# Kernel optimization log

Hardware: AMD Instinct MI355X
Metric: run time of the kernel (lower is better)

Reference implementation:

```python
import jax, jax.numpy as jnp
import numpy as np

B = 8192          # batch
DIM = 2048        # feature dim
FANOUT = 10       # balanced 10-ary tree, depth 3 -> 1000 leaves
N_NODES = 1 + 10 + 100  # inner nodes with classifiers = 111
NUM_CLASSES = 1000


def setup_inputs() -> dict:
    key = jax.random.key(0)
    k1, k2, k3, k4 = jax.random.split(key, 4)
    x = jax.random.normal(k1, (B, DIM), dtype=jnp.float32)
    labels = jax.random.randint(k2, (B,), 0, NUM_CLASSES, dtype=jnp.int64 if jax.config.jax_enable_x64 else jnp.int32)
    # Stacked per-node Linear(dim, num_child+1): column 0 is the extra slot
    # included in the softmax but never routed to (children use cols 1..FANOUT).
    W = jax.random.normal(k3, (N_NODES, DIM, FANOUT + 1), dtype=jnp.float32) * (1.0 / np.sqrt(DIM))
    b = jax.random.normal(k4, (N_NODES, FANOUT + 1), dtype=jnp.float32) * 0.01
    return {"x": x, "labels": labels, "W": W, "b": b}


def reference(x, labels, W, b):
    # All 111 tiny per-node Linear+softmax classifiers fused into one batched GEMM.
    logits = jnp.einsum('bd,ndk->bnk', x, W) + b          # [B, 111, 11]
    probs = jax.nn.softmax(logits, axis=-1)               # softmax over num_child+1 (incl. dummy col 0)
    # Hierarchical path probabilities (root.path_prob = 1.0):
    # level-1 nodes are children of root (node 0), via softmax columns 1..10.
    p1 = probs[:, 0, 1:]                                   # [B, 10]
    # level-2 nodes: children of nodes 1..10
    p2 = (p1[:, :, None] * probs[:, 1:11, 1:]).reshape(x.shape[0], 100)    # [B, 100]
    # leaves: children of nodes 11..110 -> 1000 classes (out[:, 1:] slice already applied)
    out = (p2[:, :, None] * probs[:, 11:111, 1:]).reshape(x.shape[0], NUM_CLASSES)  # [B, 1000]
    penalty = jnp.float32(0.0)
    return (out, penalty)
```

## Files before the change

kernel.cpp:

```cpp
#include <hip/hip_runtime.h>
#include <hip/hip_bf16.h>
#include <hip/hip_fp16.h>

typedef _Float16 f16;
typedef __attribute__((ext_vector_type(4))) _Float16 f16x4;
typedef __attribute__((ext_vector_type(8))) _Float16 f16x8;
typedef __attribute__((ext_vector_type(4))) float f32x4;

#define DIM     2048
#define BROWS   8192
#define NCOLS   1221
#define NPAD    1280
#define NNODES  111
#define BM      128
#define BN      128
#define BK      32

__global__ void prep_b(const float* __restrict__ W, f16* __restrict__ Bt) {
    int idx = blockIdx.x * 256 + threadIdx.x;
    int c  = idx >> 8;
    int d0 = (idx & 255) * 8;
    f16x8 v;
    if (c < NCOLS) {
        int n = c / 11, k = c - n * 11;
        const float* src = W + (size_t)n * DIM * 11 + k;
        #pragma unroll
        for (int e = 0; e < 8; ++e) v[e] = (f16)src[(size_t)(d0 + e) * 11];
    } else {
        #pragma unroll
        for (int e = 0; e < 8; ++e) v[e] = (f16)0.f;
    }
    *(f16x8*)(Bt + (size_t)c * DIM + d0) = v;
}

__global__ __launch_bounds__(256, 2) void gemm_f16(const float* __restrict__ X,
                                                   const f16* __restrict__ Bt,
                                                   float* __restrict__ L) {
    __shared__ f16 As[BM * BK];
    __shared__ f16 Bs[BN * BK];

    int bid = blockIdx.x;
    int swz = (bid & 7) * 80 + (bid >> 3);
    int mt = swz / 10, nt = swz - mt * 10;
    int m0 = mt * BM, n0 = nt * BN;

    int t = threadIdx.x;
    int w = t >> 6, l = t & 63;
    int r = l & 15, q = l >> 4;
    int wm = w >> 1, wn = w & 1;

    f32x4 acc[4][4];
    #pragma unroll
    for (int i = 0; i < 4; ++i)
        #pragma unroll
        for (int j = 0; j < 4; ++j) acc[i][j] = (f32x4)0.f;

    int a_row = t >> 3;
    int a_col = (t & 7) * 4;
    const float* xbase = X + (size_t)(m0 + a_row) * DIM + a_col;
    int b_row = w * 16 + (l >> 2);
    int b_off = (l & 3) * 8;
    const f16* btbase = Bt + (size_t)(n0 + b_row) * DIM + b_off;
    f16* bs_base = Bs + w * 512;

    for (int kt = 0; kt < DIM / BK; ++kt) {
        __syncthreads();
        #pragma unroll
        for (int p = 0; p < 2; ++p) {
            __builtin_amdgcn_global_load_lds(
                (const __attribute__((address_space(1))) void*)(btbase + (size_t)p * 64 * DIM + kt * BK),
                (__attribute__((address_space(3))) void*)(bs_base + p * 2048),
                16, 0, 0);
        }
        #pragma unroll
        for (int p = 0; p < 4; ++p) {
            f32x4 v = *(const f32x4*)(xbase + (size_t)p * 32 * DIM + kt * BK);
            f16x4 h; h[0] = (f16)v[0]; h[1] = (f16)v[1]; h[2] = (f16)v[2]; h[3] = (f16)v[3];
            *(f16x4*)(As + (a_row + p * 32) * BK + a_col) = h;
        }
        __syncthreads();
        f16x8 af[4], bf[4];
        #pragma unroll
        for (int m = 0; m < 4; ++m) af[m] = *(const f16x8*)(As + (wm * 64 + m * 16 + r) * BK + q * 8);
        #pragma unroll
        for (int n = 0; n < 4; ++n) bf[n] = *(const f16x8*)(Bs + (wn * 64 + n * 16 + r) * BK + q * 8);
        #pragma unroll
        for (int m = 0; m < 4; ++m)
            #pragma unroll
            for (int n = 0; n < 4; ++n)
                acc[m][n] = __builtin_amdgcn_mfma_f32_16x16x32_f16(af[m], bf[n], acc[m][n], 0, 0, 0);
    }

    #pragma unroll
    for (int m = 0; m < 4; ++m) {
        int row = m0 + wm * 64 + m * 16 + q * 4;
        #pragma unroll
        for (int n = 0; n < 4; ++n) {
            int col = n0 + wn * 64 + n * 16 + r;
            #pragma unroll
            for (int j = 0; j < 4; ++j)
                L[(size_t)(row + j) * NPAD + col] = acc[m][n][j];
        }
    }
}

__global__ void tree_epi(const float* __restrict__ L, const float* __restrict__ bias,
                         float* __restrict__ out) {
    __shared__ float P[4][NNODES * 11];
    int w = threadIdx.x >> 6, l = threadIdx.x & 63;
    int row = blockIdx.x * 4 + w;
    const float* Lr = L + (size_t)row * NPAD;

    for (int n = l; n < NNODES; n += 64) {
        float v[11], mx = -1e30f;
        #pragma unroll
        for (int k = 0; k < 11; ++k) { v[k] = Lr[n * 11 + k] + bias[n * 11 + k]; mx = fmaxf(mx, v[k]); }
        float s = 0.f;
        #pragma unroll
        for (int k = 0; k < 11; ++k) { v[k] = __expf(v[k] - mx); s += v[k]; }
        float inv = 1.f / s;
        #pragma unroll
        for (int k = 0; k < 11; ++k) P[w][n * 11 + k] = v[k] * inv;
    }
    __syncthreads();
    const float* Pw = P[w];
    for (int c = l; c < 1000; c += 64) {
        int i  = c / 100;
        int j  = (c % 100) / 10;
        int mm = c % 10;
        float p = Pw[1 + i] * Pw[(1 + i) * 11 + 1 + j] * Pw[(11 + 10 * i + j) * 11 + 1 + mm];
        out[(size_t)row * 1000 + c] = p;
    }
    if (row == 0 && threadIdx.x == 0) out[(size_t)BROWS * 1000] = 0.f;
}

extern "C" void kernel_launch(void* const* d_in, const int* in_sizes, int n_in,
                              void* d_out, int out_size, void* d_ws, size_t ws_size,
                              hipStream_t stream) {
    const float* x    = (const float*)d_in[0];
    const float* W    = (const float*)d_in[2];
    const float* bias = (const float*)d_in[3];
    float* out = (float*)d_out;

    f16*   Bt = (f16*)d_ws;
    float* L  = (float*)((char*)d_ws + (size_t)NPAD * DIM * sizeof(f16));

    prep_b  <<<NPAD, 256, 0, stream>>>(W, Bt);
    gemm_f16<<<(BROWS / BM) * (NPAD / BN), 256, 0, stream>>>(x, Bt, L);
    tree_epi<<<BROWS / 4, 256, 0, stream>>>(L, bias, out);
}
```

Baseline: 94.20 us.

## Double-buffer GEMM LDS tiles and pre-swizzle B into MFMA fragment order

The GEMM now keeps two LDS buffers for the A and B tiles. The next k-tile's global loads, including the async B load into LDS, are issued before the MFMAs on the current tile, which removes one barrier per iteration. prep_b now writes B in a fragment-major layout, so each wave's 16-byte loads are contiguous and LDS fragment reads are linear per lane. A is also stored in fragment order. The cost is twice the LDS per block and more registers held across the MFMA block for the prefetched A values, which could hurt the occupancy target of 2 blocks.

```diff
diff --git a/kernel.cpp b/kernel.cpp
--- a/kernel.cpp
+++ b/kernel.cpp
@@ -15,39 +15,48 @@
 #define BM      128
 #define BN      128
 #define BK      32
+#define NKT     (DIM / BK)
 
-__global__ void prep_b(const float* __restrict__ W, f16* __restrict__ Bt) {
+__global__ void prep_b(const float* __restrict__ W, f16* __restrict__ Bf) {
     int idx = blockIdx.x * 256 + threadIdx.x;
-    int c  = idx >> 8;
-    int d0 = (idx & 255) * 8;
+    int l  = idx & 63;
+    int g  = (idx >> 6) & 7;
+    int kt = (idx >> 9) & 63;
+    int nt = idx >> 15;
+    int r = l & 15, q = l >> 4;
+    int col = nt * 128 + g * 16 + r;
+    int d0  = kt * 32 + q * 8;
     f16x8 v;
-    if (c < NCOLS) {
-        int n = c / 11, k = c - n * 11;
-        const float* src = W + (size_t)n * DIM * 11 + k;
+    if (col < NCOLS) {
+        int n = col / 11, k = col - n * 11;
+        const float* src = W + ((size_t)n * DIM + d0) * 11 + k;
         #pragma unroll
-        for (int e = 0; e < 8; ++e) v[e] = (f16)src[(size_t)(d0 + e) * 11];
+        for (int e = 0; e < 8; ++e) v[e] = (f16)src[(size_t)e * 11];
     } else {
         #pragma unroll
         for (int e = 0; e < 8; ++e) v[e] = (f16)0.f;
     }
-    *(f16x8*)(Bt + (size_t)c * DIM + d0) = v;
+    *(f16x8*)(Bf + (size_t)idx * 8) = v;
 }
 
 __global__ __launch_bounds__(256, 2) void gemm_f16(const float* __restrict__ X,
-                                                   const f16* __restrict__ Bt,
+                                                   const f16* __restrict__ Bf,
                                                    float* __restrict__ L) {
-    __shared__ f16 As[BM * BK];
-    __shared__ f16 Bs[BN * BK];
+    __shared__ __align__(16) f16 As[2][4096];
+    __shared__ __align__(16) f16 Bs[2][4096];
 
     int bid = blockIdx.x;
     int swz = (bid & 7) * 80 + (bid >> 3);
     int mt = swz / 10, nt = swz - mt * 10;
-    int m0 = mt * BM, n0 = nt * BN;
 
     int t = threadIdx.x;
     int w = t >> 6, l = t & 63;
     int r = l & 15, q = l >> 4;
     int wm = w >> 1, wn = w & 1;
+
+    const float* a_src0 = X + (size_t)(mt * 128 + w * 16 + r) * DIM + q * 8;
+    const float* a_src1 = a_src0 + (size_t)64 * DIM;
+    const f16* b_base = Bf + (size_t)(nt * 64) * 4096;
 
     f32x4 acc[4][4];
     #pragma unroll
@@ -55,48 +64,81 @@
         #pragma unroll
         for (int j = 0; j < 4; ++j) acc[i][j] = (f32x4)0.f;
 
-    int a_row = t >> 3;
-    int a_col = (t & 7) * 4;
-    const float* xbase = X + (size_t)(m0 + a_row) * DIM + a_col;
-    int b_row = w * 16 + (l >> 2);
-    int b_off = (l & 3) * 8;
-    const f16* btbase = Bt + (size_t)(n0 + b_row) * DIM + b_off;
-    f16* bs_base = Bs + w * 512;
+#define STAGE_B(KT, CB)                                                          \
+    {                                                                            \
+        const f16* bs = b_base + (size_t)(KT) * 4096;                            \
+        _Pragma("unroll")                                                        \
+        for (int p = 0; p < 2; ++p) {                                            \
+            __builtin_amdgcn_global_load_lds(                                    \
+                (const __attribute__((address_space(1))) void*)(bs + (p*4 + w) * 512 + l * 8), \
+                (__attribute__((address_space(3))) void*)(&Bs[CB][(p*4 + w) * 512]),           \
+                16, 0, 0);                                                       \
+        }                                                                        \
+    }
 
-    for (int kt = 0; kt < DIM / BK; ++kt) {
-        __syncthreads();
+    STAGE_B(0, 0)
+    {
+        f32x4 va0 = *(const f32x4*)(a_src0);
+        f32x4 va1 = *(const f32x4*)(a_src0 + 4);
+        f32x4 va2 = *(const f32x4*)(a_src1);
+        f32x4 va3 = *(const f32x4*)(a_src1 + 4);
+        f16x8 h0, h1;
         #pragma unroll
-        for (int p = 0; p < 2; ++p) {
-            __builtin_amdgcn_global_load_lds(
-                (const __attribute__((address_space(1))) void*)(btbase + (size_t)p * 64 * DIM + kt * BK),
-                (__attribute__((address_space(3))) void*)(bs_base + p * 2048),
-                16, 0, 0);
-        }
-        #pragma unroll
-        for (int p = 0; p < 4; ++p) {
-            f32x4 v = *(const f32x4*)(xbase + (size_t)p * 32 * DIM + kt * BK);
-            f16x4 h; h[0] = (f16)v[0]; h[1] = (f16)v[1]; h[2] = (f16)v[2]; h[3] = (f16)v[3];
-            *(f16x4*)(As + (a_row + p * 32) * BK + a_col) = h;
-        }
-        __syncthreads();
+        for (int e = 0; e < 4; ++e) { h0[e] = (f16)va0[e]; h0[e+4] = (f16)va1[e];
+                                      h1[e] = (f16)va2[e]; h1[e+4] = (f16)va3[e]; }
+        *(f16x8*)(&As[0][(w * 64 + l) * 8])       = h0;
+        *(f16x8*)(&As[0][((w + 4) * 64 + l) * 8]) = h1;
+    }
+    __syncthreads();
+
+    int c = 0;
+    for (int kt = 0; kt < NKT - 1; ++kt) {
+        const float* s0 = a_src0 + (size_t)(kt + 1) * BK;
+        const float* s1 = a_src1 + (size_t)(kt + 1) * BK;
+        f32x4 va0 = *(const f32x4*)(s0);
+        f32x4 va1 = *(const f32x4*)(s0 + 4);
+        f32x4 va2 = *(const f32x4*)(s1);
+        f32x4 va3 = *(const f32x4*)(s1 + 4);
+        STAGE_B(kt + 1, c ^ 1)
         f16x8 af[4], bf[4];
         #pragma unroll
-        for (int m = 0; m < 4; ++m) af[m] = *(const f16x8*)(As + (wm * 64 + m * 16 + r) * BK + q * 8);
+        for (int m = 0; m < 4; ++m) af[m] = *(const f16x8*)(&As[c][((wm*4 + m) * 64 + l) * 8]);
         #pragma unroll
-        for (int n = 0; n < 4; ++n) bf[n] = *(const f16x8*)(Bs + (wn * 64 + n * 16 + r) * BK + q * 8);
+        for (int n = 0; n < 4; ++n) bf[n] = *(const f16x8*)(&Bs[c][((wn*4 + n) * 64 + l) * 8]);
+        #pragma unroll
+        for (int m = 0; m < 4; ++m)
+            #pragma unroll
+            for (int n = 0; n < 4; ++n)
+                acc[m][n] = __builtin_amdgcn_mfma_f32_16x16x32_f16(af[m], bf[n], acc[m][n], 0, 0, 0);
+        f16x8 h0, h1;
+        #pragma unroll
+        for (int e = 0; e < 4; ++e) { h0[e] = (f16)va0[e]; h0[e+4] = (f16)va1[e];
+                                      h1[e] = (f16)va2[e]; h1[e+4] = (f16)va3[e]; }
+        *(f16x8*)(&As[c ^ 1][(w * 64 + l) * 8])       = h0;
+        *(f16x8*)(&As[c ^ 1][((w + 4) * 64 + l) * 8]) = h1;
+        __syncthreads();
+        c ^= 1;
+    }
+    {
+        f16x8 af[4], bf[4];
+        #pragma unroll
+        for (int m = 0; m < 4; ++m) af[m] = *(const f16x8*)(&As[c][((wm*4 + m) * 64 + l) * 8]);
+        #pragma unroll
+        for (int n = 0; n < 4; ++n) bf[n] = *(const f16x8*)(&Bs[c][((wn*4 + n) * 64 + l) * 8]);
         #pragma unroll
         for (int m = 0; m < 4; ++m)
             #pragma unroll
             for (int n = 0; n < 4; ++n)
                 acc[m][n] = __builtin_amdgcn_mfma_f32_16x16x32_f16(af[m], bf[n], acc[m][n], 0, 0, 0);
     }
+#undef STAGE_B
 
     #pragma unroll
     for (int m = 0; m < 4; ++m) {
-        int row = m0 + wm * 64 + m * 16 + q * 4;
+        int row = mt * 128 + wm * 64 + m * 16 + q * 4;
         #pragma unroll
         for (int n = 0; n < 4; ++n) {
-            int col = n0 + wn * 64 + n * 16 + r;
+            int col = nt * 128 + wn * 64 + n * 16 + r;
             #pragma unroll
             for (int j = 0; j < 4; ++j)
                 L[(size_t)(row + j) * NPAD + col] = acc[m][n][j];
@@ -142,10 +184,10 @@
     const float* bias = (const float*)d_in[3];
     float* out = (float*)d_out;
 
-    f16*   Bt = (f16*)d_ws;
+    f16*   Bf = (f16*)d_ws;
     float* L  = (float*)((char*)d_ws + (size_t)NPAD * DIM * sizeof(f16));
 
-    prep_b  <<<NPAD, 256, 0, stream>>>(W, Bt);
-    gemm_f16<<<(BROWS / BM) * (NPAD / BN), 256, 0, stream>>>(x, Bt, L);
+    prep_b  <<<NPAD, 256, 0, stream>>>(W, Bf);
+    gemm_f16<<<(BROWS / BM) * (NPAD / BN), 256, 0, stream>>>(x, Bf, L);
     tree_epi<<<BROWS / 4, 256, 0, stream>>>(L, bias, out);
 }
```

Result: slower. 134.1 us (+42.4%).

## Pre-pack X and W into MFMA fragment tiles, widen BK, store logits in fp16

Applied to the files above, without the earlier changes.

Adds a prep_x kernel that converts x to fp16 and reorders it into per-tile MFMA fragment order. prep_b now writes W in the same tiled layout, so the GEMM loads both operands straight into LDS with global_load_lds and reads fragments without bank-conflicting strides. BK doubles to 64, which halves the number of barrier pairs, and the intermediate logits are stored as fp16 to cut write and read traffic. The cost is an extra pass over x (64 MB read, 32 MB write), a larger workspace, and fp16 rounding of the logits before softmax.

```diff
diff --git a/kernel.cpp b/kernel.cpp
--- a/kernel.cpp
+++ b/kernel.cpp
@@ -3,7 +3,6 @@
 #include <hip/hip_fp16.h>
 
 typedef _Float16 f16;
-typedef __attribute__((ext_vector_type(4))) _Float16 f16x4;
 typedef __attribute__((ext_vector_type(8))) _Float16 f16x8;
 typedef __attribute__((ext_vector_type(4))) float f32x4;
 
@@ -14,40 +13,74 @@
 #define NNODES  111
 #define BM      128
 #define BN      128
-#define BK      32
+#define BK      64
+#define NKT     (DIM / BK)
+#define MT      (BROWS / BM)
+#define NT      (NPAD / BN)
 
-__global__ void prep_b(const float* __restrict__ W, f16* __restrict__ Bt) {
+__global__ __launch_bounds__(256) void prep_x(const float* __restrict__ X,
+                                              f16* __restrict__ Xf) {
+    __shared__ float T[128 * 68];
+    int blk = blockIdx.x;
+    int mt = blk >> 5, kt = blk & 31;
+    int t = threadIdx.x;
+    int row = t >> 1, half = t & 1;
+    const float* src = X + (size_t)(mt * 128 + row) * DIM + kt * 64 + half * 32;
+    float* dst = T + row * 68 + half * 32;
+    #pragma unroll
+    for (int i = 0; i < 8; ++i) ((f32x4*)dst)[i] = ((const f32x4*)src)[i];
+    __syncthreads();
+    int w = t >> 6, l = t & 63, r = l & 15, q = l >> 4;
+    f16* out = Xf + (size_t)blk * 8192;
+    #pragma unroll
+    for (int p = 0; p < 4; ++p) {
+        int gk = p * 4 + w;
+        int kk = gk >> 3, g = gk & 7;
+        const float* s = T + (g * 16 + r) * 68 + kk * 32 + q * 8;
+        f32x4 a = *(const f32x4*)s;
+        f32x4 b = *(const f32x4*)(s + 4);
+        f16x8 h;
+        h[0] = (f16)a[0]; h[1] = (f16)a[1]; h[2] = (f16)a[2]; h[3] = (f16)a[3];
+        h[4] = (f16)b[0]; h[5] = (f16)b[1]; h[6] = (f16)b[2]; h[7] = (f16)b[3];
+        *(f16x8*)(out + (size_t)(p * 256 + t) * 8) = h;
+    }
+}
+
+__global__ void prep_b(const float* __restrict__ W, f16* __restrict__ Bf) {
     int idx = blockIdx.x * 256 + threadIdx.x;
-    int c  = idx >> 8;
-    int d0 = (idx & 255) * 8;
+    int c = idx & 1023, img = idx >> 10;
+    int nt = img >> 5, kt = img & 31;
+    int kk = c >> 9, g = (c >> 6) & 7, l = c & 63, r = l & 15, q = l >> 4;
+    int col = nt * 128 + g * 16 + r;
+    int d0  = kt * 64 + kk * 32 + q * 8;
     f16x8 v;
-    if (c < NCOLS) {
-        int n = c / 11, k = c - n * 11;
-        const float* src = W + (size_t)n * DIM * 11 + k;
+    if (col < NCOLS) {
+        int n = col / 11, k = col - n * 11;
+        const float* src = W + ((size_t)n * DIM + d0) * 11 + k;
         #pragma unroll
-        for (int e = 0; e < 8; ++e) v[e] = (f16)src[(size_t)(d0 + e) * 11];
+        for (int e = 0; e < 8; ++e) v[e] = (f16)src[(size_t)e * 11];
     } else {
         #pragma unroll
         for (int e = 0; e < 8; ++e) v[e] = (f16)0.f;
     }
-    *(f16x8*)(Bt + (size_t)c * DIM + d0) = v;
+    *(f16x8*)(Bf + (size_t)idx * 8) = v;
 }
 
-__global__ __launch_bounds__(256, 2) void gemm_f16(const float* __restrict__ X,
-                                                   const f16* __restrict__ Bt,
-                                                   float* __restrict__ L) {
-    __shared__ f16 As[BM * BK];
-    __shared__ f16 Bs[BN * BK];
+__global__ __launch_bounds__(256) void gemm_f16(const f16* __restrict__ Xf,
+                                                const f16* __restrict__ Bf,
+                                                f16* __restrict__ Lh) {
+    __shared__ __align__(16) f16 As[8192];
+    __shared__ __align__(16) f16 Bs[8192];
 
     int bid = blockIdx.x;
     int swz = (bid & 7) * 80 + (bid >> 3);
     int mt = swz / 10, nt = swz - mt * 10;
-    int m0 = mt * BM, n0 = nt * BN;
 
-    int t = threadIdx.x;
-    int w = t >> 6, l = t & 63;
-    int r = l & 15, q = l >> 4;
+    int t = threadIdx.x, w = t >> 6, l = t & 63, r = l & 15, q = l >> 4;
     int wm = w >> 1, wn = w & 1;
+
+    const f16* abase = Xf + (size_t)(mt * 32) * 8192 + (size_t)t * 8;
+    const f16* bbase = Bf + (size_t)(nt * 32) * 8192 + (size_t)t * 8;
 
     f32x4 acc[4][4];
     #pragma unroll
@@ -55,66 +88,63 @@
         #pragma unroll
         for (int j = 0; j < 4; ++j) acc[i][j] = (f32x4)0.f;
 
-    int a_row = t >> 3;
-    int a_col = (t & 7) * 4;
-    const float* xbase = X + (size_t)(m0 + a_row) * DIM + a_col;
-    int b_row = w * 16 + (l >> 2);
-    int b_off = (l & 3) * 8;
-    const f16* btbase = Bt + (size_t)(n0 + b_row) * DIM + b_off;
-    f16* bs_base = Bs + w * 512;
-
-    for (int kt = 0; kt < DIM / BK; ++kt) {
+    for (int kt = 0; kt < NKT; ++kt) {
+        __syncthreads();
+        const f16* asrc = abase + (size_t)kt * 8192;
+        const f16* bsrc = bbase + (size_t)kt * 8192;
+        #pragma unroll
+        for (int p = 0; p < 4; ++p) {
+            __builtin_amdgcn_global_load_lds(
+                (const __attribute__((address_space(1))) void*)(asrc + p * 2048),
+                (__attribute__((address_space(3))) void*)(As + p * 2048 + w * 512),
+                16, 0, 0);
+            __builtin_amdgcn_global_load_lds(
+                (const __attribute__((address_space(1))) void*)(bsrc + p * 2048),
+                (__attribute__((address_space(3))) void*)(Bs + p * 2048 + w * 512),
+                16, 0, 0);
+        }
         __syncthreads();
         #pragma unroll
-        for (int p = 0; p < 2; ++p) {
-            __builtin_amdgcn_global_load_lds(
-                (const __attribute__((address_space(1))) void*)(btbase + (size_t)p * 64 * DIM + kt * BK),
-                (__attribute__((address_space(3))) void*)(bs_base + p * 2048),
-                16, 0, 0);
-        }
-        #pragma unroll
-        for (int p = 0; p < 4; ++p) {
-            f32x4 v = *(const f32x4*)(xbase + (size_t)p * 32 * DIM + kt * BK);
-            f16x4 h; h[0] = (f16)v[0]; h[1] = (f16)v[1]; h[2] = (f16)v[2]; h[3] = (f16)v[3];
-            *(f16x4*)(As + (a_row + p * 32) * BK + a_col) = h;
-        }
-        __syncthreads();
-        f16x8 af[4], bf[4];
-        #pragma unroll
-        for (int m = 0; m < 4; ++m) af[m] = *(const f16x8*)(As + (wm * 64 + m * 16 + r) * BK + q * 8);
-        #pragma unroll
-        for (int n = 0; n < 4; ++n) bf[n] = *(const f16x8*)(Bs + (wn * 64 + n * 16 + r) * BK + q * 8);
-        #pragma unroll
-        for (int m = 0; m < 4; ++m)
+        for (int kk = 0; kk < 2; ++kk) {
+            f16x8 af[4], bf[4];
+            #pragma unroll
+            for (int m = 0; m < 4; ++m)
+                af[m] = *(const f16x8*)(As + ((size_t)((kk * 8 + wm * 4 + m) * 64 + l)) * 8);
             #pragma unroll
             for (int n = 0; n < 4; ++n)
-                acc[m][n] = __builtin_amdgcn_mfma_f32_16x16x32_f16(af[m], bf[n], acc[m][n], 0, 0, 0);
+                bf[n] = *(const f16x8*)(Bs + ((size_t)((kk * 8 + wn * 4 + n) * 64 + l)) * 8);
+            #pragma unroll
+            for (int m = 0; m < 4; ++m)
+                #pragma unroll
+                for (int n = 0; n < 4; ++n)
+                    acc[m][n] = __builtin_amdgcn_mfma_f32_16x16x32_f16(af[m], bf[n], acc[m][n], 0, 0, 0);
+        }
     }
 
     #pragma unroll
     for (int m = 0; m < 4; ++m) {
-        int row = m0 + wm * 64 + m * 16 + q * 4;
+        int row = mt * 128 + wm * 64 + m * 16 + q * 4;
         #pragma unroll
         for (int n = 0; n < 4; ++n) {
-            int col = n0 + wn * 64 + n * 16 + r;
+            int col = nt * 128 + wn * 64 + n * 16 + r;
             #pragma unroll
             for (int j = 0; j < 4; ++j)
-                L[(size_t)(row + j) * NPAD + col] = acc[m][n][j];
+                Lh[(size_t)(row + j) * NPAD + col] = (f16)acc[m][n][j];
         }
     }
 }
 
-__global__ void tree_epi(const float* __restrict__ L, const float* __restrict__ bias,
+__global__ void tree_epi(const f16* __restrict__ L, const float* __restrict__ bias,
                          float* __restrict__ out) {
     __shared__ float P[4][NNODES * 11];
     int w = threadIdx.x >> 6, l = threadIdx.x & 63;
     int row = blockIdx.x * 4 + w;
-    const float* Lr = L + (size_t)row * NPAD;
+    const f16* Lr = L + (size_t)row * NPAD;
 
     for (int n = l; n < NNODES; n += 64) {
         float v[11], mx = -1e30f;
         #pragma unroll
-        for (int k = 0; k < 11; ++k) { v[k] = Lr[n * 11 + k] + bias[n * 11 + k]; mx = fmaxf(mx, v[k]); }
+        for (int k = 0; k < 11; ++k) { v[k] = (float)Lr[n * 11 + k] + bias[n * 11 + k]; mx = fmaxf(mx, v[k]); }
         float s = 0.f;
         #pragma unroll
         for (int k = 0; k < 11; ++k) { v[k] = __expf(v[k] - mx); s += v[k]; }
@@ -142,10 +172,12 @@
     const float* bias = (const float*)d_in[3];
     float* out = (float*)d_out;
 
-    f16*   Bt = (f16*)d_ws;
-    float* L  = (float*)((char*)d_ws + (size_t)NPAD * DIM * sizeof(f16));
+    f16* Xf = (f16*)d_ws;
+    f16* Bf = (f16*)((char*)d_ws + 33554432);
+    f16* Lh = (f16*)((char*)d_ws + 38797312);
 
-    prep_b  <<<NPAD, 256, 0, stream>>>(W, Bt);
-    gemm_f16<<<(BROWS / BM) * (NPAD / BN), 256, 0, stream>>>(x, Bt, L);
-    tree_epi<<<BROWS / 4, 256, 0, stream>>>(L, bias, out);
+    prep_x <<<MT * NKT, 256, 0, stream>>>(x, Xf);
+    prep_b <<<1280, 256, 0, stream>>>(W, Bf);
+    gemm_f16<<<MT * NT, 256, 0, stream>>>(Xf, Bf, Lh);
+    tree_epi<<<BROWS / 4, 256, 0, stream>>>(Lh, bias, out);
 }
```

Measured after the change: 90.09 us. 4.4% less time.
